# Kernel optimization log

Measured on AMD Instinct MI355X. Metric: run time of the kernel, lower is better.

Reference implementation:

```python
import jax, jax.numpy as jnp
import numpy as np
from jax import lax

# RelationSimplestBlock(dim=256, heads=8): k_dim=v_dim=256, DV=32 per head, hidden=4*dim=1024.
B, N, D = 8, 1024, 256
H, DV = 8, 32
KD = D            # k_dim
HID = 4 * D       # RN hidden dim


def _ln(t, g, b, eps=1e-5):
    m = jnp.mean(t, axis=-1, keepdims=True)
    v = jnp.mean((t - m) ** 2, axis=-1, keepdims=True)  # biased var (torch LayerNorm)
    return (t - m) * lax.rsqrt(v + eps) * g + b


def setup_inputs() -> dict:
    key = jax.random.key(0)
    ks = jax.random.split(key, 6)
    std = 0.02
    return {
        'x': jax.random.normal(ks[0], (B, N, D), jnp.float32),
        'w_q': jax.random.normal(ks[1], (D, KD // H), jnp.float32) * std,   # impartial q head
        'w_kv': jax.random.normal(ks[2], (D, KD + D), jnp.float32) * std,
        'ln_out_g': jnp.ones((D,), jnp.float32),
        'ln_out_b': jnp.zeros((D,), jnp.float32),
        'ln_rel_g': jnp.ones((DV,), jnp.float32),
        'ln_rel_b': jnp.zeros((DV,), jnp.float32),
        'w_down': jax.random.normal(ks[3], (D, DV), jnp.float32) * std,
        'b_down': jnp.zeros((DV,), jnp.float32),
        'w_inner': jax.random.normal(ks[4], (2 * DV, HID), jnp.float32) * std,
        'b_inner': jnp.zeros((HID,), jnp.float32),
        'w_outer': jax.random.normal(ks[5], (HID, D), jnp.float32) * std,
        'b_outer': jnp.zeros((D,), jnp.float32),
    }


def reference(x, w_q, w_kv, ln_out_g, ln_out_b, ln_rel_g, ln_rel_b,
              w_down, b_down, w_inner, b_inner, w_outer, b_outer):
    pre = _ln(x, ln_out_g, ln_out_b)                                   # [B,N,D]
    # Relation (training branch): shared single query head (impartial_q_head)
    q = pre @ w_q                                                      # [B,N,DV]
    kv = pre @ w_kv                                                    # [B,N,KD+D]
    k = kv[..., :KD].reshape(B, N, H, DV).transpose(0, 2, 1, 3)        # [B,H,N,DV]
    v = kv[..., KD:].reshape(B, N, H, DV).transpose(0, 2, 1, 3)        # [B,H,N,DV]
    scores = jnp.einsum('bid,bhjd->bhij', q * (DV ** -0.5), k)         # [B,H,N,N]
    w = jax.nn.softmax(scores, axis=-1)
    soft = jnp.einsum('bhij,bhjd->bhid', w, v)                         # soft attention
    idx = jnp.argmax(w, axis=-1)                                       # [B,H,N] hard select
    hard = jnp.take_along_axis(v, jnp.broadcast_to(idx[..., None], (B, H, N, DV)), axis=2)
    rtn = soft - lax.stop_gradient(soft - hard)                        # straight-through
    rel = rtn.transpose(0, 2, 1, 3).reshape(B * N, H, DV)              # head-wise objects
    head_wise = _ln(rel, ln_rel_g, ln_rel_b)
    residual = (x @ w_down + b_down).reshape(B * N, 1, DV)             # downsampled context
    # RN (inner_depth=0, outer_depth=0): pair each head with the single context object
    pairs = jnp.concatenate([head_wise, jnp.broadcast_to(residual, (B * N, H, DV))], -1)
    inner = pairs @ w_inner + b_inner                                  # [BN,H,HID]
    mid = jax.nn.gelu(inner.sum(axis=1), approximate=False)            # sum over pairs
    out = mid @ w_outer + b_outer                                      # [BN,D]
    return out.reshape(B, N, D) + x
```

## Files before the change

### kernel.cpp

```cpp
#include <hip/hip_runtime.h>
#include <math.h>

#define D_    256
#define N_    1024
#define B_    8
#define H_    8
#define DV_   32
#define HID_  1024
#define ROWS_ (B_*N_)

typedef _Float16 f16;
typedef __attribute__((ext_vector_type(8))) _Float16 f16x8;
typedef __attribute__((ext_vector_type(4))) _Float16 f16x4;
typedef __attribute__((ext_vector_type(8))) short s16x8;
typedef __attribute__((ext_vector_type(4))) float f32x4;

#define LO_SCALE   2048.0f
#define INV_LO     (1.0f/2048.0f)
#define INV_LO2    (1.0f/4194304.0f)

__device__ __forceinline__ unsigned short f2bf(float f) {
    unsigned u = __float_as_uint(f);
    unsigned r = (u + 0x7fffu + ((u >> 16) & 1u)) >> 16;
    return (unsigned short)r;
// ... 8 lines not shown
    float y = ((((1.061405429f * t - 1.453152027f) * t + 1.421413741f) * t
                - 0.284496736f) * t + 0.254829592f) * t;
    float e = __expf(-ax * ax);
    float r = 1.f - y * e;
    return x < 0.f ? -r : r;
}
__device__ __forceinline__ float gelu(float v) {
    return 0.5f * v * (1.f + erf_fast(v * 0.70710678118f));
}

__global__ __launch_bounds__(256) void k_ln(const float* __restrict__ x,
        const float* __restrict__ g, const float* __restrict__ b,
        float* __restrict__ pre, unsigned short* __restrict__ pbf) {
    int t = threadIdx.x;
    int lane = t & 63;
    int row = blockIdx.x * 4 + (t >> 6);
    const float4 v = ((const float4*)(x + row * D_))[lane];
    float s  = v.x + v.y + v.z + v.w;
    float sq = v.x*v.x + v.y*v.y + v.z*v.z + v.w*v.w;
    #pragma unroll
    for (int o = 32; o; o >>= 1) { s += __shfl_xor(s, o); sq += __shfl_xor(sq, o); }
    float m   = s * (1.0f / D_);
    float var = sq * (1.0f / D_) - m * m;
    float rs  = rsqrtf(var + 1e-5f);
    const float4 gv = ((const float4*)g)[lane];
    const float4 bv = ((const float4*)b)[lane];
    float4 o;
    o.x = (v.x - m) * rs * gv.x + bv.x;
    o.y = (v.y - m) * rs * gv.y + bv.y;
    o.z = (v.z - m) * rs * gv.z + bv.z;
    o.w = (v.w - m) * rs * gv.w + bv.w;
    ((float4*)(pre + row * D_))[lane] = o;
    ushort4 u4;
    u4.x = f2bf(o.x); u4.y = f2bf(o.y); u4.z = f2bf(o.z); u4.w = f2bf(o.w);
    *(ushort4*)(pbf + (size_t)row * D_ + lane * 4) = u4;
}

__global__ __launch_bounds__(256) void k_gemm(const float* __restrict__ A,
        const float* __restrict__ Bm, const float* __restrict__ bias,
        float* __restrict__ C, int Ncols) {
    __shared__ float As[16][64];
    __shared__ float Bs[16][64];
    int t = threadIdx.x;
    int nBase = blockIdx.x * 64, rowBase = blockIdx.y * 64;
    int tx = t & 15, ty = t >> 4;
    int arow = t >> 2, ak = (t & 3) * 4;
    int bk = t >> 4, bn = (t & 15) * 4;
    float acc[4][4] = {};
    for (int kt = 0; kt < 256; kt += 16) {
        float4 av = *(const float4*)(A + (rowBase + arow) * 256 + kt + ak);
        As[ak+0][arow] = av.x; As[ak+1][arow] = av.y;
        As[ak+2][arow] = av.z; As[ak+3][arow] = av.w;
        float4 bv = make_float4(0.f, 0.f, 0.f, 0.f);
        if (nBase + bn < Ncols)
            bv = *(const float4*)(Bm + (kt + bk) * Ncols + nBase + bn);
        *(float4*)&Bs[bk][bn] = bv;
        __syncthreads();
        #pragma unroll
        for (int kk = 0; kk < 16; ++kk) {
            float4 a4 = *(const float4*)&As[kk][ty*4];
            float4 b4 = *(const float4*)&Bs[kk][tx*4];
            acc[0][0] += a4.x*b4.x; acc[0][1] += a4.x*b4.y; acc[0][2] += a4.x*b4.z; acc[0][3] += a4.x*b4.w;
            acc[1][0] += a4.y*b4.x; acc[1][1] += a4.y*b4.y; acc[1][2] += a4.y*b4.z; acc[1][3] += a4.y*b4.w;
            acc[2][0] += a4.z*b4.x; acc[2][1] += a4.z*b4.y; acc[2][2] += a4.z*b4.z; acc[2][3] += a4.z*b4.w;
            acc[3][0] += a4.w*b4.x; acc[3][1] += a4.w*b4.y; acc[3][2] += a4.w*b4.z; acc[3][3] += a4.w*b4.w;
        }
        __syncthreads();
    }
    int col = nBase + tx * 4;
    if (col < Ncols) {
        float4 bb = make_float4(0.f,0.f,0.f,0.f);
        if (bias) bb = *(const float4*)(bias + col);
        #pragma unroll
        for (int i = 0; i < 4; ++i) {
            float4 o;
            o.x = acc[i][0] + bb.x; o.y = acc[i][1] + bb.y;
            o.z = acc[i][2] + bb.z; o.w = acc[i][3] + bb.w;
            *(float4*)(C + (rowBase + ty*4 + i) * Ncols + col) = o;
        }
    }
}

__global__ __launch_bounds__(256) void k_gemmK(const float* __restrict__ A,
        const float* __restrict__ Bm, f16* __restrict__ khi, f16* __restrict__ klo) {
    __shared__ float As[16][64];
    __shared__ float Bs[16][64];
    int t = threadIdx.x;
    int nBase = blockIdx.x * 64, rowBase = blockIdx.y * 64;
    int tx = t & 15, ty = t >> 4;
    int arow = t >> 2, ak = (t & 3) * 4;
    int bk = t >> 4, bn = (t & 15) * 4;
    float acc[4][4] = {};
    for (int kt = 0; kt < 256; kt += 16) {
        float4 av = *(const float4*)(A + (rowBase + arow) * 256 + kt + ak);
        As[ak+0][arow] = av.x; As[ak+1][arow] = av.y;
        As[ak+2][arow] = av.z; As[ak+3][arow] = av.w;
        float4 bv = *(const float4*)(Bm + (size_t)(kt + bk) * 512 + nBase + bn);
        *(float4*)&Bs[bk][bn] = bv;
        __syncthreads();
        #pragma unroll
        for (int kk = 0; kk < 16; ++kk) {
            float4 a4 = *(const float4*)&As[kk][ty*4];
            float4 b4 = *(const float4*)&Bs[kk][tx*4];
            acc[0][0] += a4.x*b4.x; acc[0][1] += a4.x*b4.y; acc[0][2] += a4.x*b4.z; acc[0][3] += a4.x*b4.w;
            acc[1][0] += a4.y*b4.x; acc[1][1] += a4.y*b4.y; acc[1][2] += a4.y*b4.z; acc[1][3] += a4.y*b4.w;
            acc[2][0] += a4.z*b4.x; acc[2][1] += a4.z*b4.y; acc[2][2] += a4.z*b4.z; acc[2][3] += a4.z*b4.w;
            acc[3][0] += a4.w*b4.x; acc[3][1] += a4.w*b4.y; acc[3][2] += a4.w*b4.z; acc[3][3] += a4.w*b4.w;
        }
        __syncthreads();
    }
    int col = nBase + tx * 4;
    #pragma unroll
    for (int i = 0; i < 4; ++i) {
        int row = rowBase + ty * 4 + i;
        f16x4 hv, lv;
        #pragma unroll
        for (int c = 0; c < 4; ++c) {
            float v = acc[i][c];
            f16 h = (f16)v;
            hv[c] = h;
            lv[c] = (f16)((v - (float)h) * LO_SCALE);
        }
        *(f16x4*)(khi + (size_t)row * 256 + col) = hv;
        *(f16x4*)(klo + (size_t)row * 256 + col) = lv;
    }
}

__global__ __launch_bounds__(256) void k_gemmV(const unsigned short* __restrict__ A,
        const unsigned short* __restrict__ Bt, unsigned short* __restrict__ V) {
    __shared__ __align__(16) unsigned short As[2][4096];
    __shared__ __align__(16) unsigned short Bs[2][4096];
    int t = threadIdx.x;
    int rowBase = blockIdx.x * 64, colBase = blockIdx.y * 64;
    int l = t & 63, w = t >> 6, wr = w >> 1, wc = w & 1;
    int r0 = t >> 3,        c0 = t & 7;
    int r1 = (t + 256) >> 3, c1 = t & 7;
    int s0 = (r0 * 8 + (c0 ^ (r0 & 7))) * 8;
    int s1 = (r1 * 8 + (c1 ^ (r1 & 7))) * 8;
    f32x4 acc00 = {0.f,0.f,0.f,0.f}, acc01 = acc00, acc10 = acc00, acc11 = acc00;
    int m = l & 15, g = l >> 4;
    int swm = m & 7;
    {
        uint4 va0 = *(const uint4*)(A  + (size_t)(rowBase + r0) * 256 + c0 * 8);
        uint4 va1 = *(const uint4*)(A  + (size_t)(rowBase + r1) * 256 + c1 * 8);
        uint4 vb0 = *(const uint4*)(Bt + (size_t)(colBase + r0) * 256 + c0 * 8);
        uint4 vb1 = *(const uint4*)(Bt + (size_t)(colBase + r1) * 256 + c1 * 8);
        *(uint4*)&As[0][s0] = va0; *(uint4*)&As[0][s1] = va1;
        *(uint4*)&Bs[0][s0] = vb0; *(uint4*)&Bs[0][s1] = vb1;
    }
    __syncthreads();
    int cur = 0;
    for (int kt = 0; kt < 4; ++kt) {
        uint4 va0, va1, vb0, vb1;
        bool pf = (kt + 1) < 4;
        if (pf) {
            int k0 = (kt + 1) * 64;
            va0 = *(const uint4*)(A  + (size_t)(rowBase + r0) * 256 + k0 + c0 * 8);
            va1 = *(const uint4*)(A  + (size_t)(rowBase + r1) * 256 + k0 + c1 * 8);
            vb0 = *(const uint4*)(Bt + (size_t)(colBase + r0) * 256 + k0 + c0 * 8);
            vb1 = *(const uint4*)(Bt + (size_t)(colBase + r1) * 256 + k0 + c1 * 8);
        }
        #pragma unroll
        for (int ks = 0; ks < 2; ++ks) {
            int kc = ks * 4 + g;
            int sc = kc ^ swm;
            s16x8 a0 = *(const s16x8*)&As[cur][((wr*32      + m) * 8 + sc) * 8];
            s16x8 a1 = *(const s16x8*)&As[cur][((wr*32 + 16 + m) * 8 + sc) * 8];
            s16x8 b0 = *(const s16x8*)&Bs[cur][((wc*32      + m) * 8 + sc) * 8];
            s16x8 b1 = *(const s16x8*)&Bs[cur][((wc*32 + 16 + m) * 8 + sc) * 8];
            acc00 = __builtin_amdgcn_mfma_f32_16x16x32_bf16(a0, b0, acc00, 0, 0, 0);
            acc01 = __builtin_amdgcn_mfma_f32_16x16x32_bf16(a0, b1, acc01, 0, 0, 0);
            acc10 = __builtin_amdgcn_mfma_f32_16x16x32_bf16(a1, b0, acc10, 0, 0, 0);
            acc11 = __builtin_amdgcn_mfma_f32_16x16x32_bf16(a1, b1, acc11, 0, 0, 0);
        }
        if (pf) {
            *(uint4*)&As[cur ^ 1][s0] = va0; *(uint4*)&As[cur ^ 1][s1] = va1;
            *(uint4*)&Bs[cur ^ 1][s0] = vb0; *(uint4*)&Bs[cur ^ 1][s1] = vb1;
        }
        __syncthreads();
        cur ^= 1;
    }
    #pragma unroll
    for (int fr = 0; fr < 2; ++fr) {
        #pragma unroll
        for (int fc = 0; fc < 2; ++fc) {
            f32x4 Acc = fr == 0 ? (fc == 0 ? acc00 : acc01)
                                : (fc == 0 ? acc10 : acc11);
            int col = colBase + wc * 32 + fc * 16 + m;
            #pragma unroll
            for (int rr = 0; rr < 4; ++rr) {
                int row = rowBase + wr * 32 + fr * 16 + g * 4 + rr;
                V[(size_t)row * 256 + col] = f2bf(Acc[rr]);
            }
        }
    }
}

__global__ __launch_bounds__(256) void k_argmax(const float* __restrict__ q,
        const f16* __restrict__ khi_g, const f16* __restrict__ klo_g,
        int* __restrict__ idx) {
    __shared__ float mval[2][64];
    __shared__ int   midx[2][64];
    int t = threadIdx.x;
    int bid = blockIdx.x;
    int itile = bid >> 6, grp = bid & 63;
    int h = grp & 7, b = grp >> 3;
    int i0 = itile * 64;
    int w = t >> 6, l = t & 63, m = l & 15, g = l >> 4;
    int iw = w & 1, jh = w >> 1;
    int ibase = i0 + iw * 32;
    f16x8 qh0, ql0, qh1, ql1;
    {
        const float* qp0 = q + (size_t)(b * N_ + ibase + m) * 32 + g * 8;
        const float* qp1 = qp0 + 16 * 32;
        #pragma unroll
        for (int kk = 0; kk < 8; ++kk) {
            float v0 = qp0[kk]; f16 h0 = (f16)v0;
            qh0[kk] = h0; ql0[kk] = (f16)((v0 - (float)h0) * LO_SCALE);
            float v1 = qp1[kk]; f16 h1 = (f16)v1;
            qh1[kk] = h1; ql1[kk] = (f16)((v1 - (float)h1) * LO_SCALE);
        }
    }
    const f16* ph = khi_g + (size_t)(b * N_ + jh * 512 + m) * 256 + h * 32 + g * 8;
    const f16* pl = klo_g + (size_t)(b * N_ + jh * 512 + m) * 256 + h * 32 + g * 8;
    float best0[4] = {-3e38f, -3e38f, -3e38f, -3e38f};
    float best1[4] = {-3e38f, -3e38f, -3e38f, -3e38f};
    int   bj0[4] = {0,0,0,0}, bj1[4] = {0,0,0,0};
    f16x8 bh = *(const f16x8*)ph;
    f16x8 bl = *(const f16x8*)pl;
    #pragma unroll 2
    for (int jt = 0; jt < 32; ++jt) {
        f16x8 nh, nl;
        if (jt < 31) {
            nh = *(const f16x8*)(ph + (size_t)(jt + 1) * 4096);
            nl = *(const f16x8*)(pl + (size_t)(jt + 1) * 4096);
        }
        f32x4 z = {0.f, 0.f, 0.f, 0.f};
        f32x4 ah0 = __builtin_amdgcn_mfma_f32_16x16x32_f16(qh0, bh, z, 0, 0, 0);
        f32x4 ax0 = __builtin_amdgcn_mfma_f32_16x16x32_f16(qh0, bl, z, 0, 0, 0);
        ax0 = __builtin_amdgcn_mfma_f32_16x16x32_f16(ql0, bh, ax0, 0, 0, 0);
        f32x4 al0 = __builtin_amdgcn_mfma_f32_16x16x32_f16(ql0, bl, z, 0, 0, 0);
        f32x4 ah1 = __builtin_amdgcn_mfma_f32_16x16x32_f16(qh1, bh, z, 0, 0, 0);
        f32x4 ax1 = __builtin_amdgcn_mfma_f32_16x16x32_f16(qh1, bl, z, 0, 0, 0);
        ax1 = __builtin_amdgcn_mfma_f32_16x16x32_f16(ql1, bh, ax1, 0, 0, 0);
        f32x4 al1 = __builtin_amdgcn_mfma_f32_16x16x32_f16(ql1, bl, z, 0, 0, 0);
        int jg = jh * 512 + jt * 16 + m;
        #pragma unroll
        for (int r = 0; r < 4; ++r) {
            float s0 = ah0[r] + ax0[r] * INV_LO + al0[r] * INV_LO2;
            if (s0 > best0[r]) { best0[r] = s0; bj0[r] = jg; }
            float s1 = ah1[r] + ax1[r] * INV_LO + al1[r] * INV_LO2;
            if (s1 > best1[r]) { best1[r] = s1; bj1[r] = jg; }
        }
        bh = nh; bl = nl;
    }
    #pragma unroll
    for (int off = 1; off < 16; off <<= 1) {
        #pragma unroll
        for (int r = 0; r < 4; ++r) {
            float ov = __shfl_xor(best0[r], off);
            int   oj = __shfl_xor(bj0[r], off);
            if (ov > best0[r] || (ov == best0[r] && oj < bj0[r])) {
                best0[r] = ov; bj0[r] = oj;
            }
            float ov1 = __shfl_xor(best1[r], off);
            int   oj1 = __shfl_xor(bj1[r], off);
            if (ov1 > best1[r] || (ov1 == best1[r] && oj1 < bj1[r])) {
                best1[r] = ov1; bj1[r] = oj1;
            }
        }
    }
    if (m == 0) {
        #pragma unroll
        for (int r = 0; r < 4; ++r) {
            mval[jh][iw * 32 + g * 4 + r]      = best0[r];
            midx[jh][iw * 32 + g * 4 + r]      = bj0[r];
            mval[jh][iw * 32 + 16 + g * 4 + r] = best1[r];
            midx[jh][iw * 32 + 16 + g * 4 + r] = bj1[r];
        }
    }
    __syncthreads();
    if (t < 64) {
        float v0 = mval[0][t]; int j0 = midx[0][t];
        float v1 = mval[1][t]; int j1 = midx[1][t];
        idx[(b * H_ + h) * N_ + i0 + t] = (v1 > v0) ? j1 : j0;
    }
}

__global__ __launch_bounds__(256) void k_hsum(const unsigned short* __restrict__ vbf,
        const int* __restrict__ idx, const float* __restrict__ res,
        const float* __restrict__ g, const float* __restrict__ bb,
        unsigned short* __restrict__ u) {
    __shared__ float rel[32][8][33];
    int t = threadIdx.x;
    int rowBase = blockIdx.x * 32;
    int rw = t >> 3, h = t & 7;
    int bn = rowBase + rw;
    int b = bn >> 10, i = bn & 1023;
    int j = idx[(b * H_ + h) * N_ + i];
    const uint4* src = (const uint4*)(vbf + (size_t)(b * N_ + j) * 256 + h * 32);
    float v[32];
    #pragma unroll
    for (int c = 0; c < 4; ++c) {
        uint4 uu = src[c];
        v[c*8+0] = bf2f((unsigned short)(uu.x & 0xffff));
        v[c*8+1] = bf2f((unsigned short)(uu.x >> 16));
        v[c*8+2] = bf2f((unsigned short)(uu.y & 0xffff));
        v[c*8+3] = bf2f((unsigned short)(uu.y >> 16));
        v[c*8+4] = bf2f((unsigned short)(uu.z & 0xffff));
        v[c*8+5] = bf2f((unsigned short)(uu.z >> 16));
        v[c*8+6] = bf2f((unsigned short)(uu.w & 0xffff));
        v[c*8+7] = bf2f((unsigned short)(uu.w >> 16));
    }
    float s = 0.f, sq = 0.f;
    #pragma unroll
    for (int d = 0; d < 32; ++d) { s += v[d]; sq += v[d]*v[d]; }
    float m = s * (1.f/32.f), var = sq * (1.f/32.f) - m * m;
    float rs = rsqrtf(var + 1e-5f);
    #pragma unroll
    for (int d = 0; d < 32; ++d)
        rel[rw][h][d] = (v[d] - m) * rs * g[d] + bb[d];
    __syncthreads();
    #pragma unroll
    for (int e = t; e < 1024; e += 256) {
        int r = e >> 5, d = e & 31;
        float acc = 0.f;
        #pragma unroll
        for (int hh = 0; hh < 8; ++hh) acc += rel[r][hh][d];
        u[(rowBase + r) * 64 + d]      = f2bf(acc);
        u[(rowBase + r) * 64 + 32 + d] = f2bf(8.f * res[(rowBase + r) * 32 + d]);
    }
}

__global__ __launch_bounds__(256) void k_cvtT(const float* __restrict__ src,
        unsigned short* __restrict__ dst, int srcCols, int dstCols) {
    __shared__ float t64[64][65];
    int t = threadIdx.x;
    int r0 = blockIdx.x * 64, c0 = blockIdx.y * 64;
    #pragma unroll
    for (int e = t; e < 4096; e += 256) {
        int r = e >> 6, c = e & 63;
        t64[r][c] = src[(size_t)(r0 + r) * srcCols + c0 + c];
    }
    __syncthreads();
    #pragma unroll
    for (int e = t; e < 4096; e += 256) {
        int c = e >> 6, r = e & 63;
        dst[(size_t)(c0 + c) * dstCols + r0 + r] = f2bf(t64[r][c]);
    }
}

__global__ __launch_bounds__(256) void k_mid(const unsigned short* __restrict__ u,
        const unsigned short* __restrict__ wiT, const float* __restrict__ b_inner,
        unsigned short* __restrict__ mid) {
    __shared__ __align__(16) unsigned short As[4096];
    __shared__ __align__(16) unsigned short Bs[4096];
    int t = threadIdx.x;
    int rowBase = blockIdx.x * 64, colBase = blockIdx.y * 64;
    int l = t & 63, w = t >> 6, wr = w >> 1, wc = w & 1;
    int r = t >> 2, cA = (t & 3) * 2;
    {
        uint4 a0 = *(const uint4*)(u   + (size_t)(rowBase + r) * 64 + cA * 8);
        uint4 a1 = *(const uint4*)(u   + (size_t)(rowBase + r) * 64 + cA * 8 + 8);
        uint4 b0 = *(const uint4*)(wiT + (size_t)(colBase + r) * 64 + cA * 8);
        uint4 b1 = *(const uint4*)(wiT + (size_t)(colBase + r) * 64 + cA * 8 + 8);
        *(uint4*)&As[(r * 8 + ( cA      ^ (r & 7))) * 8] = a0;
        *(uint4*)&As[(r * 8 + ((cA + 1) ^ (r & 7))) * 8] = a1;
        *(uint4*)&Bs[(r * 8 + ( cA      ^ (r & 7))) * 8] = b0;
        *(uint4*)&Bs[(r * 8 + ((cA + 1) ^ (r & 7))) * 8] = b1;
    }
    __syncthreads();
    f32x4 acc00 = {0.f,0.f,0.f,0.f}, acc01 = acc00, acc10 = acc00, acc11 = acc00;
    int m = l & 15, g = l >> 4;
    int swm = m & 7;
    #pragma unroll
    for (int ks = 0; ks < 2; ++ks) {
        int kc = ks * 4 + g;
        int sc = kc ^ swm;
        s16x8 a0 = *(const s16x8*)&As[((wr*32      + m) * 8 + sc) * 8];
        s16x8 a1 = *(const s16x8*)&As[((wr*32 + 16 + m) * 8 + sc) * 8];
        s16x8 b0 = *(const s16x8*)&Bs[((wc*32      + m) * 8 + sc) * 8];
        s16x8 b1 = *(const s16x8*)&Bs[((wc*32 + 16 + m) * 8 + sc) * 8];
// ... 35 lines not shown
    int m = l & 15, g = l >> 4;
    int swm = m & 7;
    {
        uint4 va0 = *(const uint4*)(mid + (size_t)(rowBase + r0) * 1024 + c0 * 8);
        uint4 va1 = *(const uint4*)(mid + (size_t)(rowBase + r1) * 1024 + c1 * 8);
        uint4 vb0 = *(const uint4*)(woT + (size_t)(colBase + r0) * 1024 + c0 * 8);
        uint4 vb1 = *(const uint4*)(woT + (size_t)(colBase + r1) * 1024 + c1 * 8);
        *(uint4*)&As[0][s0] = va0; *(uint4*)&As[0][s1] = va1;
        *(uint4*)&Bs[0][s0] = vb0; *(uint4*)&Bs[0][s1] = vb1;
    }
    __syncthreads();
    int cur = 0;
    for (int kt = 0; kt < 16; ++kt) {
        uint4 va0, va1, vb0, vb1;
        bool pf = (kt + 1) < 16;
        if (pf) {
            int k0 = (kt + 1) * 64;
            va0 = *(const uint4*)(mid + (size_t)(rowBase + r0) * 1024 + k0 + c0 * 8);
            va1 = *(const uint4*)(mid + (size_t)(rowBase + r1) * 1024 + k0 + c1 * 8);
            vb0 = *(const uint4*)(woT + (size_t)(colBase + r0) * 1024 + k0 + c0 * 8);
            vb1 = *(const uint4*)(woT + (size_t)(colBase + r1) * 1024 + k0 + c1 * 8);
        }
        #pragma unroll
        for (int ks = 0; ks < 2; ++ks) {
            int kc = ks * 4 + g;
            int sc = kc ^ swm;
            s16x8 a0 = *(const s16x8*)&As[cur][((wr*32      + m) * 8 + sc) * 8];
            s16x8 a1 = *(const s16x8*)&As[cur][((wr*32 + 16 + m) * 8 + sc) * 8];
            s16x8 b0 = *(const s16x8*)&Bs[cur][((wc*32      + m) * 8 + sc) * 8];
            s16x8 b1 = *(const s16x8*)&Bs[cur][((wc*32 + 16 + m) * 8 + sc) * 8];
            acc00 = __builtin_amdgcn_mfma_f32_16x16x32_bf16(a0, b0, acc00, 0, 0, 0);
            acc01 = __builtin_amdgcn_mfma_f32_16x16x32_bf16(a0, b1, acc01, 0, 0, 0);
            acc10 = __builtin_amdgcn_mfma_f32_16x16x32_bf16(a1, b0, acc10, 0, 0, 0);
            acc11 = __builtin_amdgcn_mfma_f32_16x16x32_bf16(a1, b1, acc11, 0, 0, 0);
        }
        if (pf) {
            *(uint4*)&As[cur ^ 1][s0] = va0; *(uint4*)&As[cur ^ 1][s1] = va1;
            *(uint4*)&Bs[cur ^ 1][s0] = vb0; *(uint4*)&Bs[cur ^ 1][s1] = vb1;
        }
        __syncthreads();
        cur ^= 1;
    }
    #pragma unroll
    for (int fr = 0; fr < 2; ++fr) {
        #pragma unroll
        for (int fc = 0; fc < 2; ++fc) {
            f32x4 A = fr == 0 ? (fc == 0 ? acc00 : acc01)
                              : (fc == 0 ? acc10 : acc11);
            int col = colBase + wc * 32 + fc * 16 + m;
            float bo = b_outer[col];
            #pragma unroll
            for (int rr = 0; rr < 4; ++rr) {
                int row = rowBase + wr * 32 + fr * 16 + g * 4 + rr;
                out[(size_t)row * 256 + col] = A[rr] + bo + x[(size_t)row * 256 + col];
            }
        }
    }
}

extern "C" void kernel_launch(void* const* d_in, const int* in_sizes, int n_in,
                              void* d_out, int out_size, void* d_ws, size_t ws_size,
                              hipStream_t stream) {
    const float* x        = (const float*)d_in[0];
    const float* w_q      = (const float*)d_in[1];
    const float* w_kv     = (const float*)d_in[2];
    const float* ln_out_g = (const float*)d_in[3];
    const float* ln_out_b = (const float*)d_in[4];
    const float* ln_rel_g = (const float*)d_in[5];
    const float* ln_rel_b = (const float*)d_in[6];
    const float* w_down   = (const float*)d_in[7];
    const float* b_down   = (const float*)d_in[8];
    const float* w_inner  = (const float*)d_in[9];
    const float* b_inner  = (const float*)d_in[10];
    const float* w_outer  = (const float*)d_in[11];
    const float* b_outer  = (const float*)d_in[12];
    float* out = (float*)d_out;

    float* ws = (float*)d_ws;
    float* pre = ws;
    unsigned short* pbf = (unsigned short*)(ws + 2097152);
    f16* khi = (f16*)(ws + 3145728);
    f16* klo = (f16*)(ws + 4194304);
    unsigned short* vbf = (unsigned short*)(ws + 5242880);
    float* qbuf   = ws + 6291456;
    float* resbuf = ws + 6553600;
    unsigned short* ubuf = (unsigned short*)(ws + 6815744);
    int* idxbuf = (int*)(ws + 7077888);
    unsigned short* woT = (unsigned short*)(ws + 7143424);
    unsigned short* wiT = (unsigned short*)(ws + 7274496);
    unsigned short* wvT = ubuf;
    unsigned short* mid = (unsigned short*)ws;

    k_ln<<<2048, 256, 0, stream>>>(x, ln_out_g, ln_out_b, pre, pbf);
    k_gemmK<<<dim3(4, 128), 256, 0, stream>>>(pre, w_kv, khi, klo);
    k_gemm<<<dim3(1, 128), 256, 0, stream>>>(pre, w_q, nullptr, qbuf, 32);
    k_gemm<<<dim3(1, 128), 256, 0, stream>>>(x, w_down, b_down, resbuf, 32);
    k_cvtT<<<dim3(4, 4), 256, 0, stream>>>(w_kv + 256, wvT, 512, 256);
    k_gemmV<<<dim3(128, 4), 256, 0, stream>>>(pbf, wvT, vbf);
    k_argmax<<<1024, 256, 0, stream>>>(qbuf, khi, klo, idxbuf);
    k_cvtT<<<dim3(16, 4), 256, 0, stream>>>(w_outer, woT, 256, 1024);
    k_cvtT<<<dim3(1, 16), 256, 0, stream>>>(w_inner, wiT, 1024, 64);
    k_hsum<<<256, 256, 0, stream>>>(vbf, idxbuf, resbuf, ln_rel_g, ln_rel_b, ubuf);
    k_mid<<<dim3(128, 16), 256, 0, stream>>>(ubuf, wiT, b_inner, mid);
    k_out<<<dim3(128, 4), 256, 0, stream>>>(mid, woT, b_outer, x, out);
}
```

Baseline: 151.5 us.

## Fuse q projection into K GEMM and widen argmax wave tiling over query rows

The q projection moves into the K GEMM as an extra column-block of blocks that writes q directly as hi/lo f16 split values, which removes one kernel launch and the per-block fp32-to-f16 conversion in the argmax kernel. The argmax kernel is also reorganised so each wave handles all 64 query rows against a quarter of the keys instead of 32 rows against half. Each loaded K fragment is now reused across four query subtiles, at the cost of more accumulator registers and a 4-way merge in shared memory. The extra q blocks compute a mostly zero-padded 64-wide tile, so some of their work is wasted.

```diff
diff --git a/kernel.cpp b/kernel.cpp
--- a/kernel.cpp
+++ b/kernel.cpp
@@ -114,11 +114,14 @@
 }
 
 __global__ __launch_bounds__(256) void k_gemmK(const float* __restrict__ A,
-        const float* __restrict__ Bm, f16* __restrict__ khi, f16* __restrict__ klo) {
+        const float* __restrict__ Bm, const float* __restrict__ Bq,
+        f16* __restrict__ khi, f16* __restrict__ klo,
+        f16* __restrict__ qhi, f16* __restrict__ qlo) {
     __shared__ float As[16][64];
     __shared__ float Bs[16][64];
     int t = threadIdx.x;
-    int nBase = blockIdx.x * 64, rowBase = blockIdx.y * 64;
+    int bx = blockIdx.x;
+    int nBase = bx * 64, rowBase = blockIdx.y * 64;
     int tx = t & 15, ty = t >> 4;
     int arow = t >> 2, ak = (t & 3) * 4;
     int bk = t >> 4, bn = (t & 15) * 4;
@@ -127,7 +130,11 @@
         float4 av = *(const float4*)(A + (rowBase + arow) * 256 + kt + ak);
         As[ak+0][arow] = av.x; As[ak+1][arow] = av.y;
         As[ak+2][arow] = av.z; As[ak+3][arow] = av.w;
-        float4 bv = *(const float4*)(Bm + (size_t)(kt + bk) * 512 + nBase + bn);
+        float4 bv = make_float4(0.f, 0.f, 0.f, 0.f);
+        if (bx < 4)
+            bv = *(const float4*)(Bm + (size_t)(kt + bk) * 512 + nBase + bn);
+        else if (bn < 32)
+            bv = *(const float4*)(Bq + (size_t)(kt + bk) * 32 + bn);
         *(float4*)&Bs[bk][bn] = bv;
         __syncthreads();
         #pragma unroll
@@ -141,7 +148,7 @@
         }
         __syncthreads();
     }
-    int col = nBase + tx * 4;
+    int col = tx * 4;
     #pragma unroll
     for (int i = 0; i < 4; ++i) {
         int row = rowBase + ty * 4 + i;
@@ -153,8 +160,13 @@
             hv[c] = h;
             lv[c] = (f16)((v - (float)h) * LO_SCALE);
         }
-        *(f16x4*)(khi + (size_t)row * 256 + col) = hv;
-        *(f16x4*)(klo + (size_t)row * 256 + col) = lv;
+        if (bx < 4) {
+            *(f16x4*)(khi + (size_t)row * 256 + nBase + col) = hv;
+            *(f16x4*)(klo + (size_t)row * 256 + nBase + col) = lv;
+        } else if (col < 32) {
+            *(f16x4*)(qhi + (size_t)row * 32 + col) = hv;
+            *(f16x4*)(qlo + (size_t)row * 32 + col) = lv;
+        }
     }
 }
 
@@ -228,94 +240,87 @@
     }
 }
 
-__global__ __launch_bounds__(256) void k_argmax(const float* __restrict__ q,
-        const f16* __restrict__ khi_g, const f16* __restrict__ klo_g,
-        int* __restrict__ idx) {
-    __shared__ float mval[2][64];
-    __shared__ int   midx[2][64];
+__global__ __launch_bounds__(256) void k_argmax(const f16* __restrict__ qhi_g,
+        const f16* __restrict__ qlo_g, const f16* __restrict__ khi_g,
+        const f16* __restrict__ klo_g, int* __restrict__ idx) {
+    __shared__ float mval[4][64];
+    __shared__ int   midx[4][64];
     int t = threadIdx.x;
     int bid = blockIdx.x;
     int itile = bid >> 6, grp = bid & 63;
     int h = grp & 7, b = grp >> 3;
     int i0 = itile * 64;
-    int w = t >> 6, l = t & 63, m = l & 15, g = l >> 4;
-    int iw = w & 1, jh = w >> 1;
-    int ibase = i0 + iw * 32;
-    f16x8 qh0, ql0, qh1, ql1;
-    {
-        const float* qp0 = q + (size_t)(b * N_ + ibase + m) * 32 + g * 8;
-        const float* qp1 = qp0 + 16 * 32;
-        #pragma unroll
-        for (int kk = 0; kk < 8; ++kk) {
-            float v0 = qp0[kk]; f16 h0 = (f16)v0;
-            qh0[kk] = h0; ql0[kk] = (f16)((v0 - (float)h0) * LO_SCALE);
-            float v1 = qp1[kk]; f16 h1 = (f16)v1;
-            qh1[kk] = h1; ql1[kk] = (f16)((v1 - (float)h1) * LO_SCALE);
-        }
-    }
-    const f16* ph = khi_g + (size_t)(b * N_ + jh * 512 + m) * 256 + h * 32 + g * 8;
-    const f16* pl = klo_g + (size_t)(b * N_ + jh * 512 + m) * 256 + h * 32 + g * 8;
-    float best0[4] = {-3e38f, -3e38f, -3e38f, -3e38f};
-    float best1[4] = {-3e38f, -3e38f, -3e38f, -3e38f};
-    int   bj0[4] = {0,0,0,0}, bj1[4] = {0,0,0,0};
+    int jq = t >> 6, l = t & 63, m = l & 15, g = l >> 4;
+    f16x8 qh[4], ql[4];
+    #pragma unroll
+    for (int s = 0; s < 4; ++s) {
+        qh[s] = *(const f16x8*)(qhi_g + (size_t)(b * N_ + i0 + s * 16 + m) * 32 + g * 8);
+        ql[s] = *(const f16x8*)(qlo_g + (size_t)(b * N_ + i0 + s * 16 + m) * 32 + g * 8);
+    }
+    const f16* ph = khi_g + (size_t)(b * N_ + jq * 256 + m) * 256 + h * 32 + g * 8;
+    const f16* pl = klo_g + (size_t)(b * N_ + jq * 256 + m) * 256 + h * 32 + g * 8;
+    float best[4][4];
+    int   bj[4][4];
+    #pragma unroll
+    for (int s = 0; s < 4; ++s)
+        #pragma unroll
+        for (int r = 0; r < 4; ++r) { best[s][r] = -3e38f; bj[s][r] = 0; }
     f16x8 bh = *(const f16x8*)ph;
     f16x8 bl = *(const f16x8*)pl;
     #pragma unroll 2
-    for (int jt = 0; jt < 32; ++jt) {
+    for (int jt = 0; jt < 16; ++jt) {
         f16x8 nh, nl;
-        if (jt < 31) {
+        if (jt < 15) {
             nh = *(const f16x8*)(ph + (size_t)(jt + 1) * 4096);
             nl = *(const f16x8*)(pl + (size_t)(jt + 1) * 4096);
         }
-        f32x4 z = {0.f, 0.f, 0.f, 0.f};
-        f32x4 ah0 = __builtin_amdgcn_mfma_f32_16x16x32_f16(qh0, bh, z, 0, 0, 0);
-        f32x4 ax0 = __builtin_amdgcn_mfma_f32_16x16x32_f16(qh0, bl, z, 0, 0, 0);
-        ax0 = __builtin_amdgcn_mfma_f32_16x16x32_f16(ql0, bh, ax0, 0, 0, 0);
-        f32x4 al0 = __builtin_amdgcn_mfma_f32_16x16x32_f16(ql0, bl, z, 0, 0, 0);
-        f32x4 ah1 = __builtin_amdgcn_mfma_f32_16x16x32_f16(qh1, bh, z, 0, 0, 0);
-        f32x4 ax1 = __builtin_amdgcn_mfma_f32_16x16x32_f16(qh1, bl, z, 0, 0, 0);
-        ax1 = __builtin_amdgcn_mfma_f32_16x16x32_f16(ql1, bh, ax1, 0, 0, 0);
-        f32x4 al1 = __builtin_amdgcn_mfma_f32_16x16x32_f16(ql1, bl, z, 0, 0, 0);
-        int jg = jh * 512 + jt * 16 + m;
-        #pragma unroll
-        for (int r = 0; r < 4; ++r) {
-            float s0 = ah0[r] + ax0[r] * INV_LO + al0[r] * INV_LO2;
-            if (s0 > best0[r]) { best0[r] = s0; bj0[r] = jg; }
-            float s1 = ah1[r] + ax1[r] * INV_LO + al1[r] * INV_LO2;
-            if (s1 > best1[r]) { best1[r] = s1; bj1[r] = jg; }
+        int jg = jq * 256 + jt * 16 + m;
+        #pragma unroll
+        for (int s = 0; s < 4; ++s) {
+            f32x4 z = {0.f, 0.f, 0.f, 0.f};
+            f32x4 ah = __builtin_amdgcn_mfma_f32_16x16x32_f16(qh[s], bh, z, 0, 0, 0);
+            f32x4 ax = __builtin_amdgcn_mfma_f32_16x16x32_f16(qh[s], bl, z, 0, 0, 0);
+            ax = __builtin_amdgcn_mfma_f32_16x16x32_f16(ql[s], bh, ax, 0, 0, 0);
+            f32x4 al = __builtin_amdgcn_mfma_f32_16x16x32_f16(ql[s], bl, z, 0, 0, 0);
+            #pragma unroll
+            for (int r = 0; r < 4; ++r) {
+                float sc = ah[r] + ax[r] * INV_LO + al[r] * INV_LO2;
+                if (sc > best[s][r]) { best[s][r] = sc; bj[s][r] = jg; }
+            }
         }
         bh = nh; bl = nl;
     }
     #pragma unroll
     for (int off = 1; off < 16; off <<= 1) {
         #pragma unroll
-        for (int r = 0; r < 4; ++r) {
-            float ov = __shfl_xor(best0[r], off);
-            int   oj = __shfl_xor(bj0[r], off);
-            if (ov > best0[r] || (ov == best0[r] && oj < bj0[r])) {
-                best0[r] = ov; bj0[r] = oj;
+        for (int s = 0; s < 4; ++s)
+            #pragma unroll
+            for (int r = 0; r < 4; ++r) {
+                float ov = __shfl_xor(best[s][r], off);
+                int   oj = __shfl_xor(bj[s][r], off);
+                if (ov > best[s][r] || (ov == best[s][r] && oj < bj[s][r])) {
+                    best[s][r] = ov; bj[s][r] = oj;
+                }
             }
-            float ov1 = __shfl_xor(best1[r], off);
-            int   oj1 = __shfl_xor(bj1[r], off);
-            if (ov1 > best1[r] || (ov1 == best1[r] && oj1 < bj1[r])) {
-                best1[r] = ov1; bj1[r] = oj1;
+    }
+    if (m == 0) {
+        #pragma unroll
+        for (int s = 0; s < 4; ++s)
+            #pragma unroll
+            for (int r = 0; r < 4; ++r) {
+                mval[jq][s * 16 + g * 4 + r] = best[s][r];
+                midx[jq][s * 16 + g * 4 + r] = bj[s][r];
             }
-        }
-    }
-    if (m == 0) {
-        #pragma unroll
-        for (int r = 0; r < 4; ++r) {
-            mval[jh][iw * 32 + g * 4 + r]      = best0[r];
-            midx[jh][iw * 32 + g * 4 + r]      = bj0[r];
-            mval[jh][iw * 32 + 16 + g * 4 + r] = best1[r];
-            midx[jh][iw * 32 + 16 + g * 4 + r] = bj1[r];
-        }
     }
     __syncthreads();
     if (t < 64) {
-        float v0 = mval[0][t]; int j0 = midx[0][t];
-        float v1 = mval[1][t]; int j1 = midx[1][t];
-        idx[(b * H_ + h) * N_ + i0 + t] = (v1 > v0) ? j1 : j0;
+        float v = mval[0][t]; int j = midx[0][t];
+        #pragma unroll
+        for (int q = 1; q < 4; ++q) {
+            float vq = mval[q][t]; int jjq = midx[q][t];
+            if (vq > v) { v = vq; j = jjq; }
+        }
+        idx[(b * H_ + h) * N_ + i0 + t] = j;
     }
 }
 
@@ -531,7 +536,8 @@
     f16* khi = (f16*)(ws + 3145728);
     f16* klo = (f16*)(ws + 4194304);
     unsigned short* vbf = (unsigned short*)(ws + 5242880);
-    float* qbuf   = ws + 6291456;
+    f16* qhi = (f16*)(ws + 6291456);
+    f16* qlo = (f16*)(ws + 6422528);
     float* resbuf = ws + 6553600;
     unsigned short* ubuf = (unsigned short*)(ws + 6815744);
     int* idxbuf = (int*)(ws + 7077888);
@@ -541,12 +547,11 @@
     unsigned short* mid = (unsigned short*)ws;
 
     k_ln<<<2048, 256, 0, stream>>>(x, ln_out_g, ln_out_b, pre, pbf);
-    k_gemmK<<<dim3(4, 128), 256, 0, stream>>>(pre, w_kv, khi, klo);
-    k_gemm<<<dim3(1, 128), 256, 0, stream>>>(pre, w_q, nullptr, qbuf, 32);
+    k_gemmK<<<dim3(5, 128), 256, 0, stream>>>(pre, w_kv, w_q, khi, klo, qhi, qlo);
     k_gemm<<<dim3(1, 128), 256, 0, stream>>>(x, w_down, b_down, resbuf, 32);
     k_cvtT<<<dim3(4, 4), 256, 0, stream>>>(w_kv + 256, wvT, 512, 256);
     k_gemmV<<<dim3(128, 4), 256, 0, stream>>>(pbf, wvT, vbf);
-    k_argmax<<<1024, 256, 0, stream>>>(qbuf, khi, klo, idxbuf);
+    k_argmax<<<1024, 256, 0, stream>>>(qhi, qlo, khi, klo, idxbuf);
     k_cvtT<<<dim3(16, 4), 256, 0, stream>>>(w_outer, woT, 256, 1024);
     k_cvtT<<<dim3(1, 16), 256, 0, stream>>>(w_inner, wiT, 1024, 64);
     k_hsum<<<256, 256, 0, stream>>>(vbf, idxbuf, resbuf, ln_rel_g, ln_rel_b, ubuf);
```

After: 142.0 us. 6.3% less time.

## Fuse q projection into K GEMM and deepen argmax K prefetch

Applied to the files above, without the earlier changes.

The q projection is folded into the K GEMM as an extra column block that writes q directly as hi/lo f16 pairs. This removes a separate launch and the per-block float-to-split conversion inside the argmax kernel. The argmax inner loop now keeps four K tiles in flight in registers instead of one, hiding more global-load latency. The cost is higher register pressure in argmax, and the extra GEMM block computes mostly wasted columns, since only 32 of its 64 are used.

```diff
diff --git a/kernel.cpp b/kernel.cpp
--- a/kernel.cpp
+++ b/kernel.cpp
@@ -114,11 +114,14 @@
 }
 
 __global__ __launch_bounds__(256) void k_gemmK(const float* __restrict__ A,
-        const float* __restrict__ Bm, f16* __restrict__ khi, f16* __restrict__ klo) {
+        const float* __restrict__ Bm, const float* __restrict__ Bq,
+        f16* __restrict__ khi, f16* __restrict__ klo,
+        f16* __restrict__ qhi, f16* __restrict__ qlo) {
     __shared__ float As[16][64];
     __shared__ float Bs[16][64];
     int t = threadIdx.x;
-    int nBase = blockIdx.x * 64, rowBase = blockIdx.y * 64;
+    int bx = blockIdx.x;
+    int nBase = bx * 64, rowBase = blockIdx.y * 64;
     int tx = t & 15, ty = t >> 4;
     int arow = t >> 2, ak = (t & 3) * 4;
     int bk = t >> 4, bn = (t & 15) * 4;
@@ -127,7 +130,11 @@
         float4 av = *(const float4*)(A + (rowBase + arow) * 256 + kt + ak);
         As[ak+0][arow] = av.x; As[ak+1][arow] = av.y;
         As[ak+2][arow] = av.z; As[ak+3][arow] = av.w;
-        float4 bv = *(const float4*)(Bm + (size_t)(kt + bk) * 512 + nBase + bn);
+        float4 bv = make_float4(0.f, 0.f, 0.f, 0.f);
+        if (bx < 4)
+            bv = *(const float4*)(Bm + (size_t)(kt + bk) * 512 + nBase + bn);
+        else if (bn < 32)
+            bv = *(const float4*)(Bq + (size_t)(kt + bk) * 32 + bn);
         *(float4*)&Bs[bk][bn] = bv;
         __syncthreads();
         #pragma unroll
@@ -141,7 +148,7 @@
         }
         __syncthreads();
     }
-    int col = nBase + tx * 4;
+    int col = tx * 4;
     #pragma unroll
     for (int i = 0; i < 4; ++i) {
         int row = rowBase + ty * 4 + i;
@@ -153,8 +160,13 @@
             hv[c] = h;
             lv[c] = (f16)((v - (float)h) * LO_SCALE);
         }
-        *(f16x4*)(khi + (size_t)row * 256 + col) = hv;
-        *(f16x4*)(klo + (size_t)row * 256 + col) = lv;
+        if (bx < 4) {
+            *(f16x4*)(khi + (size_t)row * 256 + nBase + col) = hv;
+            *(f16x4*)(klo + (size_t)row * 256 + nBase + col) = lv;
+        } else if (col < 32) {
+            *(f16x4*)(qhi + (size_t)row * 32 + col) = hv;
+            *(f16x4*)(qlo + (size_t)row * 32 + col) = lv;
+        }
     }
 }
 
@@ -228,9 +240,9 @@
     }
 }
 
-__global__ __launch_bounds__(256) void k_argmax(const float* __restrict__ q,
-        const f16* __restrict__ khi_g, const f16* __restrict__ klo_g,
-        int* __restrict__ idx) {
+__global__ __launch_bounds__(256) void k_argmax(const f16* __restrict__ qhi_g,
+        const f16* __restrict__ qlo_g, const f16* __restrict__ khi_g,
+        const f16* __restrict__ klo_g, int* __restrict__ idx) {
     __shared__ float mval[2][64];
     __shared__ int   midx[2][64];
     int t = threadIdx.x;
@@ -241,51 +253,69 @@
     int w = t >> 6, l = t & 63, m = l & 15, g = l >> 4;
     int iw = w & 1, jh = w >> 1;
     int ibase = i0 + iw * 32;
-    f16x8 qh0, ql0, qh1, ql1;
-    {
-        const float* qp0 = q + (size_t)(b * N_ + ibase + m) * 32 + g * 8;
-        const float* qp1 = qp0 + 16 * 32;
-        #pragma unroll
-        for (int kk = 0; kk < 8; ++kk) {
-            float v0 = qp0[kk]; f16 h0 = (f16)v0;
-            qh0[kk] = h0; ql0[kk] = (f16)((v0 - (float)h0) * LO_SCALE);
-            float v1 = qp1[kk]; f16 h1 = (f16)v1;
-            qh1[kk] = h1; ql1[kk] = (f16)((v1 - (float)h1) * LO_SCALE);
-        }
-    }
+    f16x8 qh0 = *(const f16x8*)(qhi_g + (size_t)(b * N_ + ibase + m) * 32 + g * 8);
+    f16x8 ql0 = *(const f16x8*)(qlo_g + (size_t)(b * N_ + ibase + m) * 32 + g * 8);
+    f16x8 qh1 = *(const f16x8*)(qhi_g + (size_t)(b * N_ + ibase + 16 + m) * 32 + g * 8);
+    f16x8 ql1 = *(const f16x8*)(qlo_g + (size_t)(b * N_ + ibase + 16 + m) * 32 + g * 8);
     const f16* ph = khi_g + (size_t)(b * N_ + jh * 512 + m) * 256 + h * 32 + g * 8;
     const f16* pl = klo_g + (size_t)(b * N_ + jh * 512 + m) * 256 + h * 32 + g * 8;
     float best0[4] = {-3e38f, -3e38f, -3e38f, -3e38f};
     float best1[4] = {-3e38f, -3e38f, -3e38f, -3e38f};
     int   bj0[4] = {0,0,0,0}, bj1[4] = {0,0,0,0};
-    f16x8 bh = *(const f16x8*)ph;
-    f16x8 bl = *(const f16x8*)pl;
-    #pragma unroll 2
-    for (int jt = 0; jt < 32; ++jt) {
-        f16x8 nh, nl;
-        if (jt < 31) {
-            nh = *(const f16x8*)(ph + (size_t)(jt + 1) * 4096);
-            nl = *(const f16x8*)(pl + (size_t)(jt + 1) * 4096);
-        }
-        f32x4 z = {0.f, 0.f, 0.f, 0.f};
-        f32x4 ah0 = __builtin_amdgcn_mfma_f32_16x16x32_f16(qh0, bh, z, 0, 0, 0);
-        f32x4 ax0 = __builtin_amdgcn_mfma_f32_16x16x32_f16(qh0, bl, z, 0, 0, 0);
-        ax0 = __builtin_amdgcn_mfma_f32_16x16x32_f16(ql0, bh, ax0, 0, 0, 0);
-        f32x4 al0 = __builtin_amdgcn_mfma_f32_16x16x32_f16(ql0, bl, z, 0, 0, 0);
-        f32x4 ah1 = __builtin_amdgcn_mfma_f32_16x16x32_f16(qh1, bh, z, 0, 0, 0);
-        f32x4 ax1 = __builtin_amdgcn_mfma_f32_16x16x32_f16(qh1, bl, z, 0, 0, 0);
-        ax1 = __builtin_amdgcn_mfma_f32_16x16x32_f16(ql1, bh, ax1, 0, 0, 0);
-        f32x4 al1 = __builtin_amdgcn_mfma_f32_16x16x32_f16(ql1, bl, z, 0, 0, 0);
-        int jg = jh * 512 + jt * 16 + m;
-        #pragma unroll
-        for (int r = 0; r < 4; ++r) {
-            float s0 = ah0[r] + ax0[r] * INV_LO + al0[r] * INV_LO2;
-            if (s0 > best0[r]) { best0[r] = s0; bj0[r] = jg; }
-            float s1 = ah1[r] + ax1[r] * INV_LO + al1[r] * INV_LO2;
-            if (s1 > best1[r]) { best1[r] = s1; bj1[r] = jg; }
-        }
-        bh = nh; bl = nl;
-    }
+    f16x8 h0 = *(const f16x8*)(ph);
+    f16x8 l0 = *(const f16x8*)(pl);
+    f16x8 h1 = *(const f16x8*)(ph + 4096);
+    f16x8 l1 = *(const f16x8*)(pl + 4096);
+    f16x8 h2 = *(const f16x8*)(ph + 2 * 4096);
+    f16x8 l2 = *(const f16x8*)(pl + 2 * 4096);
+    f16x8 h3 = *(const f16x8*)(ph + 3 * 4096);
+    f16x8 l3 = *(const f16x8*)(pl + 3 * 4096);
+#define PROC(BH, BL, JT)                                                        \
+    {                                                                           \
+        f32x4 z = {0.f, 0.f, 0.f, 0.f};                                         \
+        f32x4 ah0 = __builtin_amdgcn_mfma_f32_16x16x32_f16(qh0, BH, z, 0, 0, 0);\
+        f32x4 ax0 = __builtin_amdgcn_mfma_f32_16x16x32_f16(qh0, BL, z, 0, 0, 0);\
+        ax0 = __builtin_amdgcn_mfma_f32_16x16x32_f16(ql0, BH, ax0, 0, 0, 0);    \
+        f32x4 al0 = __builtin_amdgcn_mfma_f32_16x16x32_f16(ql0, BL, z, 0, 0, 0);\
+        f32x4 ah1 = __builtin_amdgcn_mfma_f32_16x16x32_f16(qh1, BH, z, 0, 0, 0);\
+        f32x4 ax1 = __builtin_amdgcn_mfma_f32_16x16x32_f16(qh1, BL, z, 0, 0, 0);\
+        ax1 = __builtin_amdgcn_mfma_f32_16x16x32_f16(ql1, BH, ax1, 0, 0, 0);    \
+        f32x4 al1 = __builtin_amdgcn_mfma_f32_16x16x32_f16(ql1, BL, z, 0, 0, 0);\
+        int jg = jh * 512 + (JT) * 16 + m;                                      \
+        _Pragma("unroll")                                                       \
+        for (int r = 0; r < 4; ++r) {                                           \
+            float s0v = ah0[r] + ax0[r] * INV_LO + al0[r] * INV_LO2;            \
+            if (s0v > best0[r]) { best0[r] = s0v; bj0[r] = jg; }                \
+            float s1v = ah1[r] + ax1[r] * INV_LO + al1[r] * INV_LO2;            \
+            if (s1v > best1[r]) { best1[r] = s1v; bj1[r] = jg; }                \
+        }                                                                       \
+    }
+    #pragma unroll 1
+    for (int jb = 0; jb < 8; ++jb) {
+        bool pf = jb < 7;
+        int jt0 = jb * 4;
+        PROC(h0, l0, jt0 + 0)
+        if (pf) {
+            h0 = *(const f16x8*)(ph + (size_t)(jt0 + 4) * 4096);
+            l0 = *(const f16x8*)(pl + (size_t)(jt0 + 4) * 4096);
+        }
+        PROC(h1, l1, jt0 + 1)
+        if (pf) {
+            h1 = *(const f16x8*)(ph + (size_t)(jt0 + 5) * 4096);
+            l1 = *(const f16x8*)(pl + (size_t)(jt0 + 5) * 4096);
+        }
+        PROC(h2, l2, jt0 + 2)
+        if (pf) {
+            h2 = *(const f16x8*)(ph + (size_t)(jt0 + 6) * 4096);
+            l2 = *(const f16x8*)(pl + (size_t)(jt0 + 6) * 4096);
+        }
+        PROC(h3, l3, jt0 + 3)
+        if (pf) {
+            h3 = *(const f16x8*)(ph + (size_t)(jt0 + 7) * 4096);
+            l3 = *(const f16x8*)(pl + (size_t)(jt0 + 7) * 4096);
+        }
+    }
+#undef PROC
     #pragma unroll
     for (int off = 1; off < 16; off <<= 1) {
         #pragma unroll
@@ -531,7 +561,8 @@
     f16* khi = (f16*)(ws + 3145728);
     f16* klo = (f16*)(ws + 4194304);
     unsigned short* vbf = (unsigned short*)(ws + 5242880);
-    float* qbuf   = ws + 6291456;
+    f16* qhi = (f16*)(ws + 6291456);
+    f16* qlo = (f16*)(ws + 6422528);
     float* resbuf = ws + 6553600;
     unsigned short* ubuf = (unsigned short*)(ws + 6815744);
     int* idxbuf = (int*)(ws + 7077888);
@@ -541,12 +572,11 @@
     unsigned short* mid = (unsigned short*)ws;
 
     k_ln<<<2048, 256, 0, stream>>>(x, ln_out_g, ln_out_b, pre, pbf);
-    k_gemmK<<<dim3(4, 128), 256, 0, stream>>>(pre, w_kv, khi, klo);
-    k_gemm<<<dim3(1, 128), 256, 0, stream>>>(pre, w_q, nullptr, qbuf, 32);
+    k_gemmK<<<dim3(5, 128), 256, 0, stream>>>(pre, w_kv, w_q, khi, klo, qhi, qlo);
     k_gemm<<<dim3(1, 128), 256, 0, stream>>>(x, w_down, b_down, resbuf, 32);
     k_cvtT<<<dim3(4, 4), 256, 0, stream>>>(w_kv + 256, wvT, 512, 256);
     k_gemmV<<<dim3(128, 4), 256, 0, stream>>>(pbf, wvT, vbf);
-    k_argmax<<<1024, 256, 0, stream>>>(qbuf, khi, klo, idxbuf);
+    k_argmax<<<1024, 256, 0, stream>>>(qhi, qlo, khi, klo, idxbuf);
     k_cvtT<<<dim3(16, 4), 256, 0, stream>>>(w_outer, woT, 256, 1024);
     k_cvtT<<<dim3(1, 16), 256, 0, stream>>>(w_inner, wiT, 1024, 64);
     k_hsum<<<256, 256, 0, stream>>>(vbf, idxbuf, resbuf, ln_rel_g, ln_rel_b, ubuf);
```

New measurement: 143.2 us. 5.5% less time.

## Split argmax key range across blocks and fuse q projection into K GEMM

Applied to the files above, without the earlier changes.

The q projection is folded into the K GEMM as a fifth column block that writes q directly as hi/lo fp16 pairs. This drops one launch and the in-kernel q split inside argmax. The argmax kernel now splits the key dimension into two halves across separate blocks, doubling the grid to 2048 blocks with half the loop length each. Partial max values and indices are written out and merged in k_hsum, which costs an extra workspace buffer and extra reads in exchange for more parallelism. The fifth GEMM block computes a mostly zero-padded tile, which wastes some compute.

```diff
diff --git a/kernel.cpp b/kernel.cpp
--- a/kernel.cpp
+++ b/kernel.cpp
@@ -114,11 +114,14 @@
 }
 
 __global__ __launch_bounds__(256) void k_gemmK(const float* __restrict__ A,
-        const float* __restrict__ Bm, f16* __restrict__ khi, f16* __restrict__ klo) {
+        const float* __restrict__ Bm, const float* __restrict__ Bq,
+        f16* __restrict__ khi, f16* __restrict__ klo,
+        f16* __restrict__ qhi, f16* __restrict__ qlo) {
     __shared__ float As[16][64];
     __shared__ float Bs[16][64];
     int t = threadIdx.x;
-    int nBase = blockIdx.x * 64, rowBase = blockIdx.y * 64;
+    int bx = blockIdx.x;
+    int nBase = bx * 64, rowBase = blockIdx.y * 64;
     int tx = t & 15, ty = t >> 4;
     int arow = t >> 2, ak = (t & 3) * 4;
     int bk = t >> 4, bn = (t & 15) * 4;
@@ -127,7 +130,11 @@
         float4 av = *(const float4*)(A + (rowBase + arow) * 256 + kt + ak);
         As[ak+0][arow] = av.x; As[ak+1][arow] = av.y;
         As[ak+2][arow] = av.z; As[ak+3][arow] = av.w;
-        float4 bv = *(const float4*)(Bm + (size_t)(kt + bk) * 512 + nBase + bn);
+        float4 bv = make_float4(0.f, 0.f, 0.f, 0.f);
+        if (bx < 4)
+            bv = *(const float4*)(Bm + (size_t)(kt + bk) * 512 + nBase + bn);
+        else if (bn < 32)
+            bv = *(const float4*)(Bq + (size_t)(kt + bk) * 32 + bn);
         *(float4*)&Bs[bk][bn] = bv;
         __syncthreads();
         #pragma unroll
@@ -141,7 +148,7 @@
         }
         __syncthreads();
     }
-    int col = nBase + tx * 4;
+    int col = tx * 4;
     #pragma unroll
     for (int i = 0; i < 4; ++i) {
         int row = rowBase + ty * 4 + i;
@@ -153,8 +160,13 @@
             hv[c] = h;
             lv[c] = (f16)((v - (float)h) * LO_SCALE);
         }
-        *(f16x4*)(khi + (size_t)row * 256 + col) = hv;
-        *(f16x4*)(klo + (size_t)row * 256 + col) = lv;
+        if (bx < 4) {
+            *(f16x4*)(khi + (size_t)row * 256 + nBase + col) = hv;
+            *(f16x4*)(klo + (size_t)row * 256 + nBase + col) = lv;
+        } else if (col < 32) {
+            *(f16x4*)(qhi + (size_t)row * 32 + col) = hv;
+            *(f16x4*)(qlo + (size_t)row * 32 + col) = lv;
+        }
     }
 }
 
@@ -228,42 +240,38 @@
     }
 }
 
-__global__ __launch_bounds__(256) void k_argmax(const float* __restrict__ q,
-        const f16* __restrict__ khi_g, const f16* __restrict__ klo_g,
-        int* __restrict__ idx) {
+__global__ __launch_bounds__(256) void k_argmax(const f16* __restrict__ qhi_g,
+        const f16* __restrict__ qlo_g, const f16* __restrict__ khi_g,
+        const f16* __restrict__ klo_g, float* __restrict__ valp,
+        int* __restrict__ idxp) {
     __shared__ float mval[2][64];
     __shared__ int   midx[2][64];
     int t = threadIdx.x;
     int bid = blockIdx.x;
-    int itile = bid >> 6, grp = bid & 63;
+    int grp = bid & 63;
+    int rest = bid >> 6;
+    int itile = rest >> 1, jh = rest & 1;
     int h = grp & 7, b = grp >> 3;
     int i0 = itile * 64;
     int w = t >> 6, l = t & 63, m = l & 15, g = l >> 4;
-    int iw = w & 1, jh = w >> 1;
+    int iw = w & 1, jq = w >> 1;
     int ibase = i0 + iw * 32;
-    f16x8 qh0, ql0, qh1, ql1;
-    {
-        const float* qp0 = q + (size_t)(b * N_ + ibase + m) * 32 + g * 8;
-        const float* qp1 = qp0 + 16 * 32;
-        #pragma unroll
-        for (int kk = 0; kk < 8; ++kk) {
-            float v0 = qp0[kk]; f16 h0 = (f16)v0;
-            qh0[kk] = h0; ql0[kk] = (f16)((v0 - (float)h0) * LO_SCALE);
-            float v1 = qp1[kk]; f16 h1 = (f16)v1;
-            qh1[kk] = h1; ql1[kk] = (f16)((v1 - (float)h1) * LO_SCALE);
-        }
-    }
-    const f16* ph = khi_g + (size_t)(b * N_ + jh * 512 + m) * 256 + h * 32 + g * 8;
-    const f16* pl = klo_g + (size_t)(b * N_ + jh * 512 + m) * 256 + h * 32 + g * 8;
+    int jbase = jh * 512 + jq * 256;
+    f16x8 qh0 = *(const f16x8*)(qhi_g + (size_t)(b * N_ + ibase + m) * 32 + g * 8);
+    f16x8 ql0 = *(const f16x8*)(qlo_g + (size_t)(b * N_ + ibase + m) * 32 + g * 8);
+    f16x8 qh1 = *(const f16x8*)(qhi_g + (size_t)(b * N_ + ibase + 16 + m) * 32 + g * 8);
+    f16x8 ql1 = *(const f16x8*)(qlo_g + (size_t)(b * N_ + ibase + 16 + m) * 32 + g * 8);
+    const f16* ph = khi_g + (size_t)(b * N_ + jbase + m) * 256 + h * 32 + g * 8;
+    const f16* pl = klo_g + (size_t)(b * N_ + jbase + m) * 256 + h * 32 + g * 8;
     float best0[4] = {-3e38f, -3e38f, -3e38f, -3e38f};
     float best1[4] = {-3e38f, -3e38f, -3e38f, -3e38f};
     int   bj0[4] = {0,0,0,0}, bj1[4] = {0,0,0,0};
     f16x8 bh = *(const f16x8*)ph;
     f16x8 bl = *(const f16x8*)pl;
     #pragma unroll 2
-    for (int jt = 0; jt < 32; ++jt) {
+    for (int jt = 0; jt < 16; ++jt) {
         f16x8 nh, nl;
-        if (jt < 31) {
+        if (jt < 15) {
             nh = *(const f16x8*)(ph + (size_t)(jt + 1) * 4096);
             nl = *(const f16x8*)(pl + (size_t)(jt + 1) * 4096);
         }
@@ -276,13 +284,13 @@
         f32x4 ax1 = __builtin_amdgcn_mfma_f32_16x16x32_f16(qh1, bl, z, 0, 0, 0);
         ax1 = __builtin_amdgcn_mfma_f32_16x16x32_f16(ql1, bh, ax1, 0, 0, 0);
         f32x4 al1 = __builtin_amdgcn_mfma_f32_16x16x32_f16(ql1, bl, z, 0, 0, 0);
-        int jg = jh * 512 + jt * 16 + m;
+        int jg = jbase + jt * 16 + m;
         #pragma unroll
         for (int r = 0; r < 4; ++r) {
-            float s0 = ah0[r] + ax0[r] * INV_LO + al0[r] * INV_LO2;
-            if (s0 > best0[r]) { best0[r] = s0; bj0[r] = jg; }
-            float s1 = ah1[r] + ax1[r] * INV_LO + al1[r] * INV_LO2;
-            if (s1 > best1[r]) { best1[r] = s1; bj1[r] = jg; }
+            float s0v = ah0[r] + ax0[r] * INV_LO + al0[r] * INV_LO2;
+            if (s0v > best0[r]) { best0[r] = s0v; bj0[r] = jg; }
+            float s1v = ah1[r] + ax1[r] * INV_LO + al1[r] * INV_LO2;
+            if (s1v > best1[r]) { best1[r] = s1v; bj1[r] = jg; }
         }
         bh = nh; bl = nl;
     }
@@ -305,31 +313,37 @@
     if (m == 0) {
         #pragma unroll
         for (int r = 0; r < 4; ++r) {
-            mval[jh][iw * 32 + g * 4 + r]      = best0[r];
-            midx[jh][iw * 32 + g * 4 + r]      = bj0[r];
-            mval[jh][iw * 32 + 16 + g * 4 + r] = best1[r];
-            midx[jh][iw * 32 + 16 + g * 4 + r] = bj1[r];
+            mval[jq][iw * 32 + g * 4 + r]      = best0[r];
+            midx[jq][iw * 32 + g * 4 + r]      = bj0[r];
+            mval[jq][iw * 32 + 16 + g * 4 + r] = best1[r];
+            midx[jq][iw * 32 + 16 + g * 4 + r] = bj1[r];
         }
     }
     __syncthreads();
     if (t < 64) {
         float v0 = mval[0][t]; int j0 = midx[0][t];
         float v1 = mval[1][t]; int j1 = midx[1][t];
-        idx[(b * H_ + h) * N_ + i0 + t] = (v1 > v0) ? j1 : j0;
+        float v = (v1 > v0) ? v1 : v0;
+        int   j = (v1 > v0) ? j1 : j0;
+        int o = (b * H_ + h) * N_ + i0 + t;
+        valp[jh * 65536 + o] = v;
+        idxp[jh * 65536 + o] = j;
     }
 }
 
 __global__ __launch_bounds__(256) void k_hsum(const unsigned short* __restrict__ vbf,
-        const int* __restrict__ idx, const float* __restrict__ res,
-        const float* __restrict__ g, const float* __restrict__ bb,
-        unsigned short* __restrict__ u) {
+        const float* __restrict__ valp, const int* __restrict__ idxp,
+        const float* __restrict__ res, const float* __restrict__ g,
+        const float* __restrict__ bb, unsigned short* __restrict__ u) {
     __shared__ float rel[32][8][33];
     int t = threadIdx.x;
     int rowBase = blockIdx.x * 32;
     int rw = t >> 3, h = t & 7;
     int bn = rowBase + rw;
     int b = bn >> 10, i = bn & 1023;
-    int j = idx[(b * H_ + h) * N_ + i];
+    int o = (b * H_ + h) * N_ + i;
+    float v0 = valp[o], v1 = valp[65536 + o];
+    int j = (v1 > v0) ? idxp[65536 + o] : idxp[o];
     const uint4* src = (const uint4*)(vbf + (size_t)(b * N_ + j) * 256 + h * 32);
     float v[32];
     #pragma unroll
@@ -531,25 +545,26 @@
     f16* khi = (f16*)(ws + 3145728);
     f16* klo = (f16*)(ws + 4194304);
     unsigned short* vbf = (unsigned short*)(ws + 5242880);
-    float* qbuf   = ws + 6291456;
+    f16* qhi = (f16*)(ws + 6291456);
+    f16* qlo = (f16*)(ws + 6422528);
     float* resbuf = ws + 6553600;
     unsigned short* ubuf = (unsigned short*)(ws + 6815744);
-    int* idxbuf = (int*)(ws + 7077888);
-    unsigned short* woT = (unsigned short*)(ws + 7143424);
-    unsigned short* wiT = (unsigned short*)(ws + 7274496);
+    float* valp = ws + 7077888;
+    int* idxp = (int*)(ws + 7208960);
+    unsigned short* woT = (unsigned short*)(ws + 7340032);
+    unsigned short* wiT = (unsigned short*)(ws + 7471104);
     unsigned short* wvT = ubuf;
     unsigned short* mid = (unsigned short*)ws;
 
     k_ln<<<2048, 256, 0, stream>>>(x, ln_out_g, ln_out_b, pre, pbf);
-    k_gemmK<<<dim3(4, 128), 256, 0, stream>>>(pre, w_kv, khi, klo);
-    k_gemm<<<dim3(1, 128), 256, 0, stream>>>(pre, w_q, nullptr, qbuf, 32);
+    k_gemmK<<<dim3(5, 128), 256, 0, stream>>>(pre, w_kv, w_q, khi, klo, qhi, qlo);
     k_gemm<<<dim3(1, 128), 256, 0, stream>>>(x, w_down, b_down, resbuf, 32);
     k_cvtT<<<dim3(4, 4), 256, 0, stream>>>(w_kv + 256, wvT, 512, 256);
     k_gemmV<<<dim3(128, 4), 256, 0, stream>>>(pbf, wvT, vbf);
-    k_argmax<<<1024, 256, 0, stream>>>(qbuf, khi, klo, idxbuf);
+    k_argmax<<<2048, 256, 0, stream>>>(qhi, qlo, khi, klo, valp, idxp);
     k_cvtT<<<dim3(16, 4), 256, 0, stream>>>(w_outer, woT, 256, 1024);
     k_cvtT<<<dim3(1, 16), 256, 0, stream>>>(w_inner, wiT, 1024, 64);
-    k_hsum<<<256, 256, 0, stream>>>(vbf, idxbuf, resbuf, ln_rel_g, ln_rel_b, ubuf);
+    k_hsum<<<256, 256, 0, stream>>>(vbf, valp, idxp, resbuf, ln_rel_g, ln_rel_b, ubuf);
     k_mid<<<dim3(128, 16), 256, 0, stream>>>(ubuf, wiT, b_inner, mid);
     k_out<<<dim3(128, 4), 256, 0, stream>>>(mid, woT, b_outer, x, out);
 }
```

Result: faster. 141.8 us (-6.4%).
